# Kernel tuning notes

Measured on AMD Instinct MI355X. Metric: run time of the kernel, lower is better.

The kernel has to match this reference:

```python
import jax, jax.numpy as jnp
import numpy as np

D = 64      # deg_dim
T = 3       # num_deg_types

def setup_inputs() -> dict:
    key = jax.random.key(0)
    ks = jax.random.split(key, 7)
    B, H, W = 4, 256, 256
    s = lambda *sh: 1.0 / np.sqrt(sh[0])
    inp = {
        "deg_features": jax.random.normal(ks[0], (B, T * D, H, W), dtype=jnp.float32),
        # graph_att: Linear(2D -> D), GELU, Linear(D -> 1), Sigmoid
        "W1": jax.random.normal(ks[1], (2 * D, D), dtype=jnp.float32) * s(2 * D),
        "b1": jax.random.normal(ks[2], (D,), dtype=jnp.float32) * 0.01,
        "W2": jax.random.normal(ks[3], (D, 1), dtype=jnp.float32) * s(D),
        "b2": jax.random.normal(ks[4], (1,), dtype=jnp.float32) * 0.01,
        # fusion: 1x1 Conv2d(T*D -> D), expressed as (T*D, D) matrix
        "Wf": jax.random.normal(ks[5], (T * D, D), dtype=jnp.float32) * s(T * D),
        "bf": jax.random.normal(ks[6], (D,), dtype=jnp.float32) * 0.01,
    }
    return inp

def reference(deg_features, W1, b1, W2, b2, Wf, bf):
    B, C, H, W = deg_features.shape
    # split channel into T blocks of D, move channels last: (B, T, H, W, D)
    x = deg_features.reshape(B, T, D, H, W).transpose(0, 1, 3, 4, 2)
    # Linear on concat([x_i, x_j]) decomposes: concat @ W1 = x_i @ W1[:D] + x_j @ W1[D:]
    a = jnp.einsum('bthwd,de->bthwe', x, W1[:D])   # contribution of i-feature
    c = jnp.einsum('bthwd,de->bthwe', x, W1[D:])   # contribution of j-feature
    outs = []
    for i in range(T):
        acc = x[:, i]  # diagonal weight is 1
        for j in range(T):
            if i == j:
                continue
            h = jax.nn.gelu(a[:, i] + c[:, j] + b1, approximate=False)  # (B,H,W,D)
            w = jax.nn.sigmoid(h @ W2 + b2)                             # (B,H,W,1)
            acc = acc + w * x[:, j]
        outs.append(acc)
    cat = jnp.stack(outs, axis=3)                  # (B,H,W,T,D)
    flat = cat.reshape(B, H, W, T * D)
    out = flat @ Wf + bf                           # 1x1 conv as matmul
    return out.transpose(0, 3, 1, 2)               # (B, D, H, W)
```

## Files before the change

### kernel.cpp

```cpp
#include <hip/hip_runtime.h>

#define HW 65536

typedef __attribute__((ext_vector_type(8))) short short8;
typedef __attribute__((ext_vector_type(4))) float f32x4;

static __device__ __forceinline__ unsigned short f2bf(float f) {
    unsigned int u = __float_as_uint(f);
    u += 0x7FFFu + ((u >> 16) & 1u);
    return (unsigned short)(u >> 16);
}
static __device__ __forceinline__ float bf2f(unsigned short s) {
    return __uint_as_float(((unsigned int)s) << 16);
}

static __device__ __forceinline__ float gelu_sig(float h) {
    float h2 = h * h;
    float z  = h * __builtin_fmaf(-0.1029392f, h2, -2.3021178f);
    float ex = __builtin_amdgcn_exp2f(z);
    return h * __builtin_amdgcn_rcpf(1.0f + ex);
}
static __device__ __forceinline__ float sigmoid_fast(float v) {
    float ex = __builtin_amdgcn_exp2f(-1.4426950f * v);
    return __builtin_amdgcn_rcpf(1.0f + ex);
}

__global__ void dig_prep(const float* __restrict__ W1, const float* __restrict__ Wf,
                         unsigned short* __restrict__ w1t, unsigned short* __restrict__ wft) {
    int tid = blockIdx.x * blockDim.x + threadIdx.x;
    int stride = gridDim.x * blockDim.x;
    for (int i = tid; i < 128 * 64; i += stride) {
        int r = i >> 6, d = i & 63;
        int kind = r >> 6, e = r & 63;
        w1t[i] = f2bf(W1[(kind * 64 + d) * 64 + e]);
    }
    for (int i = tid; i < 64 * 192; i += stride) {
        int r = i / 192, c = i - r * 192;
        wft[i] = f2bf(Wf[c * 64 + r]);
    }
}

__global__ __launch_bounds__(256, 6) void dig_main(
    const float* __restrict__ x,
    const float* __restrict__ W1,
    const float* __restrict__ b1,
    const float* __restrict__ W2,
    const float* __restrict__ b2,
    const float* __restrict__ Wf,
    const float* __restrict__ bfv,
    float* __restrict__ out,
    const unsigned short* __restrict__ w1t_g,
    const unsigned short* __restrict__ wft_g,
    int wsok)
{
    __shared__ __align__(16) unsigned short XS[32 * 200];
    __shared__ float GT[192];
    __shared__ float BW[132];

    const int tid = threadIdx.x;
    const int l   = tid & 63;
    const int w   = tid >> 6;
    const int lm  = l & 15;
    const int q   = l >> 4;

    const int tile = blockIdx.x;
    const int bb   = tile >> 11;
    const int hw0  = (tile & 2047) * 32;

    const float* xbase = x + (size_t)bb * (192 * HW) + hw0;
    for (int idx = tid; idx < 1536; idx += 256) {
        int c = idx >> 3, pg = idx & 7;
        float4 v = *(const float4*)(xbase + (size_t)c * HW + pg * 4);
        int p0 = pg * 4;
        XS[(p0 + 0) * 200 + c] = f2bf(v.x);
        XS[(p0 + 1) * 200 + c] = f2bf(v.y);
        XS[(p0 + 2) * 200 + c] = f2bf(v.z);
        XS[(p0 + 3) * 200 + c] = f2bf(v.w);
    }
    if (tid < 192)       GT[tid] = 0.f;
    if (tid < 64)        BW[tid] = b1[tid];
    else if (tid < 128)  BW[tid] = W2[tid - 64];
    else if (tid == 128) BW[128] = b2[0];
    __syncthreads();

    short8 afr[2][2];
    if (wsok) {
        #pragma unroll
        for (int kind = 0; kind < 2; ++kind)
            #pragma unroll
            for (int ks = 0; ks < 2; ++ks)
                afr[kind][ks] = *(const short8*)&w1t_g[(kind * 64 + w * 16 + lm) * 64 + ks * 32 + q * 8];
    } else {
        #pragma unroll
        for (int kind = 0; kind < 2; ++kind)
            #pragma unroll
            for (int ks = 0; ks < 2; ++ks) {
                union { short8 v; unsigned short u[8]; } tmp;
                #pragma unroll
                for (int j = 0; j < 8; ++j)
                    tmp.u[j] = f2bf(W1[(kind * 64 + ks * 32 + q * 8 + j) * 64 + (w * 16 + lm)]);
                afr[kind][ks] = tmp.v;
            }
    }

    {
        float4 b1v4 = *(const float4*)&BW[w * 16 + q * 4];
        float4 w2v4 = *(const float4*)&BW[64 + w * 16 + q * 4];
        const float b1a[4] = {b1v4.x, b1v4.y, b1v4.z, b1v4.w};
        const float w2a[4] = {w2v4.x, w2v4.y, w2v4.z, w2v4.w};

        #pragma unroll
        for (int pt = 0; pt < 2; ++pt) {
            f32x4 acc[2][3];
            #pragma unroll
            for (int kind = 0; kind < 2; ++kind)
                #pragma unroll
                for (int t = 0; t < 3; ++t)
                    acc[kind][t] = (f32x4){0.f, 0.f, 0.f, 0.f};

            #pragma unroll
            for (int t = 0; t < 3; ++t) {
                const unsigned short* xr = &XS[(pt * 16 + lm) * 200 + t * 64 + q * 8];
                short8 bfr0 = *(const short8*)xr;
                short8 bfr1 = *(const short8*)(xr + 32);
                #pragma unroll
                for (int kind = 0; kind < 2; ++kind) {
                    acc[kind][t] = __builtin_amdgcn_mfma_f32_16x16x32_bf16(
                        afr[kind][0], bfr0, acc[kind][t], 0, 0, 0);
                    acc[kind][t] = __builtin_amdgcn_mfma_f32_16x16x32_bf16(
                        afr[kind][1], bfr1, acc[kind][t], 0, 0, 0);
                }
            }

            #pragma unroll
            for (int i = 0; i < 3; ++i) {
                float ab[4];
                #pragma unroll
                for (int r = 0; r < 4; ++r) ab[r] = acc[0][i][r] + b1a[r];
                #pragma unroll
                for (int jj = 0; jj < 2; ++jj) {
                    const int j = (jj == 0) ? ((i == 0) ? 1 : 0) : ((i == 2) ? 1 : 2);
                    float p = 0.f;
                    #pragma unroll
                    for (int r = 0; r < 4; ++r) {
                        float h = ab[r] + acc[1][j][r];
                        p = __builtin_fmaf(w2a[r], gelu_sig(h), p);
                    }
                    p += __shfl_xor(p, 16);
                    p += __shfl_xor(p, 32);
                    if (l < 16) atomicAdd(&GT[(2 * i + jj) * 32 + pt * 16 + lm], p);
                }
            }
        }
    }
    __syncthreads();

    {
        const int pix = tid >> 3;
        const int cg  = tid & 7;
        unsigned short* xrow = XS + pix * 200;

        ushort4 xv[3][2];
        #pragma unroll
        for (int t = 0; t < 3; ++t)
            #pragma unroll
            for (int ch = 0; ch < 2; ++ch)
                xv[t][ch] = *(const ushort4*)&xrow[t * 64 + cg * 4 + ch * 32];

        float fx[3][2][4];
        #pragma unroll
        for (int t = 0; t < 3; ++t)
            #pragma unroll
            for (int ch = 0; ch < 2; ++ch) {
                fx[t][ch][0] = bf2f(xv[t][ch].x);
                fx[t][ch][1] = bf2f(xv[t][ch].y);
                fx[t][ch][2] = bf2f(xv[t][ch].z);
                fx[t][ch][3] = bf2f(xv[t][ch].w);
            }

        const float b2v = BW[128];
        float g[6];
        #pragma unroll
        for (int p6 = 0; p6 < 6; ++p6)
            g[p6] = sigmoid_fast(GT[p6 * 32 + pix] + b2v);

        #pragma unroll
        for (int i = 0; i < 3; ++i) {
            const int j0c = (i == 0) ? 1 : 0;
            const int j1c = (i == 2) ? 1 : 2;
            const float g0 = g[2 * i + 0];
            const float g1 = g[2 * i + 1];
            #pragma unroll
            for (int ch = 0; ch < 2; ++ch) {
                ushort4 o;
                o.x = f2bf(__builtin_fmaf(g1, fx[j1c][ch][0], __builtin_fmaf(g0, fx[j0c][ch][0], fx[i][ch][0])));
                o.y = f2bf(__builtin_fmaf(g1, fx[j1c][ch][1], __builtin_fmaf(g0, fx[j0c][ch][1], fx[i][ch][1])));
                o.z = f2bf(__builtin_fmaf(g1, fx[j1c][ch][2], __builtin_fmaf(g0, fx[j0c][ch][2], fx[i][ch][2])));
                o.w = f2bf(__builtin_fmaf(g1, fx[j1c][ch][3], __builtin_fmaf(g0, fx[j0c][ch][3], fx[i][ch][3])));
                *(ushort4*)&xrow[i * 64 + cg * 4 + ch * 32] = o;
            }
        }
    }
    __syncthreads();

    {
        const int mt  = w >> 1;
        const int ntb = (w & 1) * 2;
        f32x4 eacc[2];
        eacc[0] = (f32x4){0.f, 0.f, 0.f, 0.f};
        eacc[1] = (f32x4){0.f, 0.f, 0.f, 0.f};
        #pragma unroll
        for (int ks = 0; ks < 6; ++ks) {
            short8 af = *(const short8*)&XS[(mt * 16 + lm) * 200 + ks * 32 + q * 8];
            #pragma unroll
            for (int ntl = 0; ntl < 2; ++ntl) {
                short8 bw8;
                if (wsok) {
                    bw8 = *(const short8*)&wft_g[((ntb + ntl) * 16 + lm) * 192 + ks * 32 + q * 8];
                } else {
                    union { short8 v; unsigned short u[8]; } tmp;
                    #pragma unroll
                    for (int j = 0; j < 8; ++j)
                        tmp.u[j] = f2bf(Wf[(ks * 32 + q * 8 + j) * 64 + (ntb + ntl) * 16 + lm]);
                    bw8 = tmp.v;
                }
                eacc[ntl] = __builtin_amdgcn_mfma_f32_16x16x32_bf16(af, bw8, eacc[ntl], 0, 0, 0);
            }
        }
        #pragma unroll
        for (int ntl = 0; ntl < 2; ++ntl) {
            int o = (ntb + ntl) * 16 + lm;
            float bo = bfv[o];
            float* obase = out + (size_t)bb * (64 * HW) + (size_t)o * HW + hw0 + mt * 16 + q * 4;
            *(float4*)obase = make_float4(eacc[ntl][0] + bo, eacc[ntl][1] + bo,
                                          eacc[ntl][2] + bo, eacc[ntl][3] + bo);
        }
    }
}

extern "C" void kernel_launch(void* const* d_in, const int* in_sizes, int n_in,
                              void* d_out, int out_size, void* d_ws, size_t ws_size,
                              hipStream_t stream) {
    (void)in_sizes; (void)n_in; (void)out_size;
    const float* x  = (const float*)d_in[0];
    const float* W1 = (const float*)d_in[1];
    const float* b1 = (const float*)d_in[2];
    const float* W2 = (const float*)d_in[3];
    const float* b2 = (const float*)d_in[4];
    const float* Wf = (const float*)d_in[5];
    const float* bf = (const float*)d_in[6];
    float* out = (float*)d_out;

    unsigned short* w1t = (unsigned short*)d_ws;
    unsigned short* wft = w1t + 128 * 64;
    const size_t need = (size_t)(128 * 64 + 64 * 192) * sizeof(unsigned short);
    int wsok = (d_ws != nullptr && ws_size >= need) ? 1 : 0;

    if (wsok) dig_prep<<<dim3(80), dim3(256), 0, stream>>>(W1, Wf, w1t, wft);
    dig_main<<<dim3(8192), dim3(256), 0, stream>>>(x, W1, b1, W2, b2, Wf, bf, out,
                                                   w1t, wft, wsok);
}
```

Before: 352.0 us.

## Double pixel tile per block and use packed bf16 conversion stores

Result: no change. 347.7 us (-1.2%).

```diff
diff --git a/kernel.cpp b/kernel.cpp
--- a/kernel.cpp
+++ b/kernel.cpp
@@ -12,6 +12,11 @@
 }
 static __device__ __forceinline__ float bf2f(unsigned short s) {
     return __uint_as_float(((unsigned int)s) << 16);
+}
+static __device__ __forceinline__ unsigned int cvt_pk_bf16(float a, float b) {
+    unsigned int r;
+    asm("v_cvt_pk_bf16_f32 %0, %1, %2" : "=v"(r) : "v"(a), "v"(b));
+    return r;
 }
 
 static __device__ __forceinline__ float gelu_sig(float h) {
@@ -53,9 +58,8 @@
     const unsigned short* __restrict__ wft_g,
     int wsok)
 {
-    __shared__ __align__(16) unsigned short XS[32 * 200];
-    __shared__ float GT[192];
-    __shared__ float BW[132];
+    __shared__ __align__(16) unsigned short XS[64 * 200];
+    __shared__ float GT[2 * 192];
 
     const int tid = threadIdx.x;
     const int l   = tid & 63;
@@ -64,24 +68,12 @@
     const int q   = l >> 4;
 
     const int tile = blockIdx.x;
-    const int bb   = tile >> 11;
-    const int hw0  = (tile & 2047) * 32;
-
-    const float* xbase = x + (size_t)bb * (192 * HW) + hw0;
-    for (int idx = tid; idx < 1536; idx += 256) {
-        int c = idx >> 3, pg = idx & 7;
-        float4 v = *(const float4*)(xbase + (size_t)c * HW + pg * 4);
-        int p0 = pg * 4;
-        XS[(p0 + 0) * 200 + c] = f2bf(v.x);
-        XS[(p0 + 1) * 200 + c] = f2bf(v.y);
-        XS[(p0 + 2) * 200 + c] = f2bf(v.z);
-        XS[(p0 + 3) * 200 + c] = f2bf(v.w);
-    }
-    if (tid < 192)       GT[tid] = 0.f;
-    if (tid < 64)        BW[tid] = b1[tid];
-    else if (tid < 128)  BW[tid] = W2[tid - 64];
-    else if (tid == 128) BW[128] = b2[0];
-    __syncthreads();
+    const int bb   = tile >> 10;
+    const int hw0  = (tile & 1023) * 64;
+
+    const float4 b1v4 = *(const float4*)(b1 + w * 16 + q * 4);
+    const float4 w2v4 = *(const float4*)(W2 + w * 16 + q * 4);
+    const float  b2v  = b2[0];
 
     short8 afr[2][2];
     if (wsok) {
@@ -103,137 +95,154 @@
             }
     }
 
+    const float* xbase = x + (size_t)bb * (192 * HW) + hw0;
+    #pragma unroll
+    for (int it = 0; it < 6; ++it) {
+        int idx = it * 256 + tid;
+        int pg = idx & 15, c = (idx >> 4) * 2;
+        const float* p0 = xbase + (size_t)c * HW + pg * 4;
+        float4 v0 = *(const float4*)p0;
+        float4 v1 = *(const float4*)(p0 + HW);
+        int px = pg * 4;
+        *(unsigned int*)&XS[(px + 0) * 200 + c] = cvt_pk_bf16(v0.x, v1.x);
+        *(unsigned int*)&XS[(px + 1) * 200 + c] = cvt_pk_bf16(v0.y, v1.y);
+        *(unsigned int*)&XS[(px + 2) * 200 + c] = cvt_pk_bf16(v0.z, v1.z);
+        *(unsigned int*)&XS[(px + 3) * 200 + c] = cvt_pk_bf16(v0.w, v1.w);
+    }
+    if (tid < 128) { GT[tid] = 0.f; GT[tid + 128] = 0.f; GT[tid + 256] = 0.f; }
+    __syncthreads();
+
     {
-        float4 b1v4 = *(const float4*)&BW[w * 16 + q * 4];
-        float4 w2v4 = *(const float4*)&BW[64 + w * 16 + q * 4];
         const float b1a[4] = {b1v4.x, b1v4.y, b1v4.z, b1v4.w};
         const float w2a[4] = {w2v4.x, w2v4.y, w2v4.z, w2v4.w};
 
         #pragma unroll
-        for (int pt = 0; pt < 2; ++pt) {
-            f32x4 acc[2][3];
-            #pragma unroll
-            for (int kind = 0; kind < 2; ++kind)
-                #pragma unroll
-                for (int t = 0; t < 3; ++t)
-                    acc[kind][t] = (f32x4){0.f, 0.f, 0.f, 0.f};
-
+        for (int st = 0; st < 2; ++st) {
+            #pragma unroll
+            for (int pt = 0; pt < 2; ++pt) {
+                f32x4 acc[2][3];
+                #pragma unroll
+                for (int kind = 0; kind < 2; ++kind)
+                    #pragma unroll
+                    for (int t = 0; t < 3; ++t)
+                        acc[kind][t] = (f32x4){0.f, 0.f, 0.f, 0.f};
+
+                #pragma unroll
+                for (int t = 0; t < 3; ++t) {
+                    const unsigned short* xr = &XS[(st * 32 + pt * 16 + lm) * 200 + t * 64 + q * 8];
+                    short8 bfr0 = *(const short8*)xr;
+                    short8 bfr1 = *(const short8*)(xr + 32);
+                    #pragma unroll
+                    for (int kind = 0; kind < 2; ++kind) {
+                        acc[kind][t] = __builtin_amdgcn_mfma_f32_16x16x32_bf16(
+                            afr[kind][0], bfr0, acc[kind][t], 0, 0, 0);
+                        acc[kind][t] = __builtin_amdgcn_mfma_f32_16x16x32_bf16(
+                            afr[kind][1], bfr1, acc[kind][t], 0, 0, 0);
+                    }
+                }
+
+                #pragma unroll
+                for (int i = 0; i < 3; ++i) {
+                    float ab[4];
+                    #pragma unroll
+                    for (int r = 0; r < 4; ++r) ab[r] = acc[0][i][r] + b1a[r];
+                    #pragma unroll
+                    for (int jj = 0; jj < 2; ++jj) {
+                        const int j = (jj == 0) ? ((i == 0) ? 1 : 0) : ((i == 2) ? 1 : 2);
+                        float p = 0.f;
+                        #pragma unroll
+                        for (int r = 0; r < 4; ++r) {
+                            float h = ab[r] + acc[1][j][r];
+                            p = __builtin_fmaf(w2a[r], gelu_sig(h), p);
+                        }
+                        p += __shfl_xor(p, 16);
+                        p += __shfl_xor(p, 32);
+                        if (l < 16) atomicAdd(&GT[st * 192 + (2 * i + jj) * 32 + pt * 16 + lm], p);
+                    }
+                }
+            }
+        }
+    }
+    __syncthreads();
+
+    {
+        const int pix = tid >> 2;
+        const int cg  = tid & 2 ? (tid & 3) : (tid & 3);
+        unsigned short* xrow = XS + pix * 200;
+
+        float g[6];
+        const float* gbase = &GT[(pix >> 5) * 192];
+        #pragma unroll
+        for (int p6 = 0; p6 < 6; ++p6)
+            g[p6] = sigmoid_fast(gbase[p6 * 32 + (pix & 31)] + b2v);
+
+        #pragma unroll
+        for (int ch = 0; ch < 4; ++ch) {
+            const int d0 = (tid & 3) * 4 + ch * 16;
+            ushort4 xv[3];
+            #pragma unroll
+            for (int t = 0; t < 3; ++t)
+                xv[t] = *(const ushort4*)&xrow[t * 64 + d0];
+            float fx[3][4];
             #pragma unroll
             for (int t = 0; t < 3; ++t) {
-                const unsigned short* xr = &XS[(pt * 16 + lm) * 200 + t * 64 + q * 8];
-                short8 bfr0 = *(const short8*)xr;
-                short8 bfr1 = *(const short8*)(xr + 32);
-                #pragma unroll
-                for (int kind = 0; kind < 2; ++kind) {
-                    acc[kind][t] = __builtin_amdgcn_mfma_f32_16x16x32_bf16(
-                        afr[kind][0], bfr0, acc[kind][t], 0, 0, 0);
-                    acc[kind][t] = __builtin_amdgcn_mfma_f32_16x16x32_bf16(
-                        afr[kind][1], bfr1, acc[kind][t], 0, 0, 0);
-                }
-            }
-
+                fx[t][0] = bf2f(xv[t].x); fx[t][1] = bf2f(xv[t].y);
+                fx[t][2] = bf2f(xv[t].z); fx[t][3] = bf2f(xv[t].w);
+            }
             #pragma unroll
             for (int i = 0; i < 3; ++i) {
-                float ab[4];
-                #pragma unroll
-                for (int r = 0; r < 4; ++r) ab[r] = acc[0][i][r] + b1a[r];
-                #pragma unroll
-                for (int jj = 0; jj < 2; ++jj) {
-                    const int j = (jj == 0) ? ((i == 0) ? 1 : 0) : ((i == 2) ? 1 : 2);
-                    float p = 0.f;
-                    #pragma unroll
-                    for (int r = 0; r < 4; ++r) {
-                        float h = ab[r] + acc[1][j][r];
-                        p = __builtin_fmaf(w2a[r], gelu_sig(h), p);
-                    }
-                    p += __shfl_xor(p, 16);
-                    p += __shfl_xor(p, 32);
-                    if (l < 16) atomicAdd(&GT[(2 * i + jj) * 32 + pt * 16 + lm], p);
-                }
+                const int j0c = (i == 0) ? 1 : 0;
+                const int j1c = (i == 2) ? 1 : 2;
+                const float g0 = g[2 * i + 0];
+                const float g1 = g[2 * i + 1];
+                float o0 = __builtin_fmaf(g1, fx[j1c][0], __builtin_fmaf(g0, fx[j0c][0], fx[i][0]));
+                float o1 = __builtin_fmaf(g1, fx[j1c][1], __builtin_fmaf(g0, fx[j0c][1], fx[i][1]));
+                float o2 = __builtin_fmaf(g1, fx[j1c][2], __builtin_fmaf(g0, fx[j0c][2], fx[i][2]));
+                float o3 = __builtin_fmaf(g1, fx[j1c][3], __builtin_fmaf(g0, fx[j0c][3], fx[i][3]));
+                uint2 ov;
+                ov.x = cvt_pk_bf16(o0, o1);
+                ov.y = cvt_pk_bf16(o2, o3);
+                *(uint2*)&xrow[i * 64 + d0] = ov;
             }
         }
-    }
-    __syncthreads();
-
-    {
-        const int pix = tid >> 3;
-        const int cg  = tid & 7;
-        unsigned short* xrow = XS + pix * 200;
-
-        ushort4 xv[3][2];
-        #pragma unroll
-        for (int t = 0; t < 3; ++t)
-            #pragma unroll
-            for (int ch = 0; ch < 2; ++ch)
-                xv[t][ch] = *(const ushort4*)&xrow[t * 64 + cg * 4 + ch * 32];
-
-        float fx[3][2][4];
-        #pragma unroll
-        for (int t = 0; t < 3; ++t)
-            #pragma unroll
-            for (int ch = 0; ch < 2; ++ch) {
-                fx[t][ch][0] = bf2f(xv[t][ch].x);
-                fx[t][ch][1] = bf2f(xv[t][ch].y);
-                fx[t][ch][2] = bf2f(xv[t][ch].z);
-                fx[t][ch][3] = bf2f(xv[t][ch].w);
-            }
-
-        const float b2v = BW[128];
-        float g[6];
-        #pragma unroll
-        for (int p6 = 0; p6 < 6; ++p6)
-            g[p6] = sigmoid_fast(GT[p6 * 32 + pix] + b2v);
-
-        #pragma unroll
-        for (int i = 0; i < 3; ++i) {
-            const int j0c = (i == 0) ? 1 : 0;
-            const int j1c = (i == 2) ? 1 : 2;
-            const float g0 = g[2 * i + 0];
-            const float g1 = g[2 * i + 1];
-            #pragma unroll
-            for (int ch = 0; ch < 2; ++ch) {
-                ushort4 o;
-                o.x = f2bf(__builtin_fmaf(g1, fx[j1c][ch][0], __builtin_fmaf(g0, fx[j0c][ch][0], fx[i][ch][0])));
-                o.y = f2bf(__builtin_fmaf(g1, fx[j1c][ch][1], __builtin_fmaf(g0, fx[j0c][ch][1], fx[i][ch][1])));
-                o.z = f2bf(__builtin_fmaf(g1, fx[j1c][ch][2], __builtin_fmaf(g0, fx[j0c][ch][2], fx[i][ch][2])));
-                o.w = f2bf(__builtin_fmaf(g1, fx[j1c][ch][3], __builtin_fmaf(g0, fx[j0c][ch][3], fx[i][ch][3])));
-                *(ushort4*)&xrow[i * 64 + cg * 4 + ch * 32] = o;
-            }
-        }
+        (void)cg;
     }
     __syncthreads();
 
     {
         const int mt  = w >> 1;
         const int ntb = (w & 1) * 2;
-        f32x4 eacc[2];
-        eacc[0] = (f32x4){0.f, 0.f, 0.f, 0.f};
-        eacc[1] = (f32x4){0.f, 0.f, 0.f, 0.f};
-        #pragma unroll
-        for (int ks = 0; ks < 6; ++ks) {
-            short8 af = *(const short8*)&XS[(mt * 16 + lm) * 200 + ks * 32 + q * 8];
+        #pragma unroll
+        for (int st = 0; st < 2; ++st) {
+            f32x4 eacc[2];
+            eacc[0] = (f32x4){0.f, 0.f, 0.f, 0.f};
+            eacc[1] = (f32x4){0.f, 0.f, 0.f, 0.f};
+            #pragma unroll
+            for (int ks = 0; ks < 6; ++ks) {
+                short8 af = *(const short8*)&XS[(st * 32 + mt * 16 + lm) * 200 + ks * 32 + q * 8];
+                #pragma unroll
+                for (int ntl = 0; ntl < 2; ++ntl) {
+                    short8 bw8;
+                    if (wsok) {
+                        bw8 = *(const short8*)&wft_g[((ntb + ntl) * 16 + lm) * 192 + ks * 32 + q * 8];
+                    } else {
+                        union { short8 v; unsigned short u[8]; } tmp;
+                        #pragma unroll
+                        for (int j = 0; j < 8; ++j)
+                            tmp.u[j] = f2bf(Wf[(ks * 32 + q * 8 + j) * 64 + (ntb + ntl) * 16 + lm]);
+                        bw8 = tmp.v;
+                    }
+                    eacc[ntl] = __builtin_amdgcn_mfma_f32_16x16x32_bf16(af, bw8, eacc[ntl], 0, 0, 0);
+                }
+            }
             #pragma unroll
             for (int ntl = 0; ntl < 2; ++ntl) {
-                short8 bw8;
-                if (wsok) {
-                    bw8 = *(const short8*)&wft_g[((ntb + ntl) * 16 + lm) * 192 + ks * 32 + q * 8];
-                } else {
-                    union { short8 v; unsigned short u[8]; } tmp;
-                    #pragma unroll
-                    for (int j = 0; j < 8; ++j)
-                        tmp.u[j] = f2bf(Wf[(ks * 32 + q * 8 + j) * 64 + (ntb + ntl) * 16 + lm]);
-                    bw8 = tmp.v;
-                }
-                eacc[ntl] = __builtin_amdgcn_mfma_f32_16x16x32_bf16(af, bw8, eacc[ntl], 0, 0, 0);
-            }
-        }
-        #pragma unroll
-        for (int ntl = 0; ntl < 2; ++ntl) {
-            int o = (ntb + ntl) * 16 + lm;
-            float bo = bfv[o];
-            float* obase = out + (size_t)bb * (64 * HW) + (size_t)o * HW + hw0 + mt * 16 + q * 4;
-            *(float4*)obase = make_float4(eacc[ntl][0] + bo, eacc[ntl][1] + bo,
-                                          eacc[ntl][2] + bo, eacc[ntl][3] + bo);
+                int o = (ntb + ntl) * 16 + lm;
+                float bo = bfv[o];
+                float* obase = out + (size_t)bb * (64 * HW) + (size_t)o * HW + hw0 + st * 32 + mt * 16 + q * 4;
+                *(float4*)obase = make_float4(eacc[ntl][0] + bo, eacc[ntl][1] + bo,
+                                              eacc[ntl][2] + bo, eacc[ntl][3] + bo);
+            }
         }
     }
 }
@@ -257,6 +266,6 @@
     int wsok = (d_ws != nullptr && ws_size >= need) ? 1 : 0;
 
     if (wsok) dig_prep<<<dim3(80), dim3(256), 0, stream>>>(W1, Wf, w1t, wft);
-    dig_main<<<dim3(8192), dim3(256), 0, stream>>>(x, W1, b1, W2, b2, Wf, bf, out,
+    dig_main<<<dim3(4096), dim3(256), 0, stream>>>(x, W1, b1, W2, b2, Wf, bf, out,
                                                    w1t, wft, wsok);
 }
```
